# Kernel tuning notes

Hardware: AMD Instinct MI355X
Metric: run time of the kernel (lower is better)

The kernel has to match this reference:

```python
import jax, jax.numpy as jnp
import numpy as np

EMBED_DIMS = 256

def setup_inputs() -> dict:
    key = jax.random.key(0)
    ks = jax.random.split(key, 6)
    C = EMBED_DIMS
    x = jax.random.normal(ks[0], (4, 2048, C), dtype=jnp.float32)
    prev_x = jax.random.normal(ks[1], (4, 2048, C), dtype=jnp.float32)
    s = 1.0 / np.sqrt(C)
    W_qkv = jax.random.uniform(ks[2], (C, 3 * C), dtype=jnp.float32, minval=-s, maxval=s)
    b_qkv = jax.random.uniform(ks[3], (3 * C,), dtype=jnp.float32, minval=-s, maxval=s)
    W_out = jax.random.uniform(ks[4], (C, C), dtype=jnp.float32, minval=-s, maxval=s)
    b_out = jax.random.uniform(ks[5], (C,), dtype=jnp.float32, minval=-s, maxval=s)
    return {"x": x, "prev_x": prev_x, "W_qkv": W_qkv, "b_qkv": b_qkv,
            "W_out": W_out, "b_out": b_out}

def reference(x, prev_x, W_qkv, b_qkv, W_out, b_out):
    B, N, C = x.shape
    xx = jnp.concatenate([prev_x, x], axis=1)          # [B, S, C], S = 2N
    qkv = xx @ W_qkv + b_qkv                            # [B, S, 3C]
    q, k, v = jnp.split(qkv, 3, axis=-1)                # each [B, S, C]
    scale = 1.0 / jnp.sqrt(jnp.asarray(C, dtype=x.dtype))
    attn = jax.nn.softmax(jnp.einsum('bqc,bkc->bqk', q, k) * scale, axis=-1)
    out = jnp.einsum('bqk,bkc->bqc', attn, v)           # [B, S, C]
    out = out @ W_out + b_out
    return out[:, -N:, :]                               # [B, N, C]
```

## Files before the change

kernel.cpp:

```cpp
#include <hip/hip_runtime.h>

typedef __bf16 bf16;
typedef __attribute__((ext_vector_type(8))) __bf16 bf16x8;
typedef __attribute__((ext_vector_type(4))) __bf16 bf16x4;
typedef __attribute__((ext_vector_type(4))) float f32x4;
typedef __attribute__((ext_vector_type(16))) float f32x16;
typedef __attribute__((ext_vector_type(4))) unsigned u32x4;

#define MFMA16(a, b, c) __builtin_amdgcn_mfma_f32_16x16x32_bf16(a, b, c, 0, 0, 0)
#define MFMA32(a, b, c) __builtin_amdgcn_mfma_f32_32x32x16_bf16(a, b, c, 0, 0, 0)

__device__ inline void gload_lds16(const void* g, void* l) {
  __builtin_amdgcn_global_load_lds(
      (const __attribute__((address_space(1))) void*)g,
      (__attribute__((address_space(3))) void*)l, 16, 0, 0);
}

__device__ inline unsigned packbf(float a, float b) {
  unsigned short x = __builtin_bit_cast(unsigned short, (bf16)a);
  unsigned short y = __builtin_bit_cast(unsigned short, (bf16)b);
  return (unsigned)x | ((unsigned)y << 16);
}

__global__ __launch_bounds__(256) void prep_w_kernel(
    const float* __restrict__ Wqkv, const float* __restrict__ Wout,
    bf16* __restrict__ Wqkvt, bf16* __restrict__ Woutt)
{
  int tid = blockIdx.x * 256 + threadIdx.x;
  int nth = gridDim.x * 256;
  for (int i = tid; i < 768 * 256; i += nth) {
    int n = i >> 8, k = i & 255;
    Wqkvt[i] = (bf16)Wqkv[k * 768 + n];
  }
  for (int i = tid; i < 256 * 256; i += nth) {
    int n = i >> 8, k = i & 255;
    Woutt[i] = (bf16)Wout[k * 256 + n];
  }
}

__global__ __launch_bounds__(256) void gemm_qkv_kernel(
    const float* __restrict__ x, const float* __restrict__ px,
    const bf16* __restrict__ Wt, const float* __restrict__ bias,
    bf16* __restrict__ Qo, bf16* __restrict__ KVo)
{
  const int idb = blockIdx.x;
  const int b = idb / 160;
  const int r = idb % 160;
  int mblk, y;
  if (r < 64) { mblk = r >> 2; y = 2 + (r & 3); }
  else { int r2 = r - 64; mblk = 16 + r2 / 6; y = r2 % 6; }
  const int bm = b * 4096 + mblk * 128;
  const int n0 = y * 128;

  const int tid = threadIdx.x;
  const int lane = tid & 63, w = tid >> 6;
  const int l15 = lane & 15, lg = lane >> 4;

  alignas(16) __shared__ bf16 Alds[128 * 32];
  alignas(16) __shared__ bf16 Wlds[128 * 32];

  f32x4 acc[2][8] = {};

  const float* xsrc = ((bm & 4095) < 2048) ? px : x;
  const size_t xbase = ((size_t)b << 19) + (size_t)(bm & 2047) * 256;

  for (int k0 = 0; k0 < 256; k0 += 32) {
    __syncthreads();
    #pragma unroll
    for (int it = 0; it < 2; it++) {
      int c = it * 256 + tid;
      int row = c >> 2, kc = (c & 3) << 3;
      const float* src = xsrc + xbase + (size_t)row * 256 + k0 + kc;
      float4 f0 = *(const float4*)src;
      float4 f1 = *(const float4*)(src + 4);
      bf16x8 v = { (bf16)f0.x, (bf16)f0.y, (bf16)f0.z, (bf16)f0.w,
                   (bf16)f1.x, (bf16)f1.y, (bf16)f1.z, (bf16)f1.w };
      *(bf16x8*)((char*)Alds + ((c << 4) ^ (((row >> 1) & 3) << 4))) = v;
    }
    #pragma unroll
    for (int jj = 0; jj < 2; jj++) {
      int j = w * 2 + jj;
      int row = j * 16 + (lane >> 2);
      int chunk = (lane & 3) ^ ((row >> 1) & 3);
      const bf16* g = Wt + (size_t)(n0 + row) * 256 + k0 + chunk * 8;
      gload_lds16(g, (char*)Wlds + j * 1024);
    }
    __syncthreads();

    const int arow0 = w * 32 + l15;
    bf16x8 af0 = *(const bf16x8*)((char*)Alds +
        (((arow0 << 6) + (lg << 4)) ^ (((arow0 >> 1) & 3) << 4)));
    const int arow1 = arow0 + 16;
    bf16x8 af1 = *(const bf16x8*)((char*)Alds +
        (((arow1 << 6) + (lg << 4)) ^ (((arow1 >> 1) & 3) << 4)));
    #pragma unroll
    for (int nt = 0; nt < 8; nt++) {
      const int wrow = nt * 16 + l15;
      bf16x8 bfr = *(const bf16x8*)((char*)Wlds +
          (((wrow << 6) + (lg << 4)) ^ (((wrow >> 1) & 3) << 4)));
      acc[0][nt] = MFMA16(af0, bfr, acc[0][nt]);
      acc[1][nt] = MFMA16(af1, bfr, acc[1][nt]);
    }
  }

  #pragma unroll
  for (int mt = 0; mt < 2; mt++) {
    #pragma unroll
    for (int nt = 0; nt < 8; nt++) {
      const int n = n0 + nt * 16 + l15;
      const float bv = bias[n];
      const int m0 = bm + w * 32 + mt * 16 + lg * 4;
      const int bq = m0 >> 12;
      const int s = m0 & 4095;
      if (n < 256) {
        if (s >= 2048) {
          const int ks = n >> 4, h2 = (n >> 3) & 1, e = n & 7;
          #pragma unroll
          for (int rr = 0; rr < 4; rr++) {
            const int qrow = bq * 2048 + (s - 2048) + rr;
            Qo[(size_t)(qrow >> 5) * 8192 + ks * 512 +
               ((qrow & 31) + 32 * h2) * 8 + e] =
                (bf16)((acc[mt][nt][rr] + bv) * 0.0625f);
          }
        }
      } else if (n < 512) {
        const int d = n - 256;
        const int ks = d >> 4, h2 = (d >> 3) & 1, e = d & 7;
        const size_t tb = (size_t)(bq * 128 + (s >> 5)) * 16384;
        #pragma unroll
        for (int rr = 0; rr < 4; rr++)
          KVo[tb + ks * 512 + (((s & 31) + rr) + 32 * h2) * 8 + e] =
              (bf16)(acc[mt][nt][rr] + bv);
      } else {
        const int d = n - 512;
        const int kv32 = s & 31;
        const int sidx = kv32 >> 4, h2 = (kv32 >> 3) & 1, e0 = kv32 & 7;
        bf16x4 st = { (bf16)(acc[mt][nt][0] + bv), (bf16)(acc[mt][nt][1] + bv),
                      (bf16)(acc[mt][nt][2] + bv), (bf16)(acc[mt][nt][3] + bv) };
        *(bf16x4*)(KVo + (size_t)(bq * 128 + (s >> 5)) * 16384 + 8192 +
                   (sidx * 8 + (d >> 5)) * 512 + ((d & 31) + 32 * h2) * 8 + e0) = st;
      }
    }
  }
}

__global__ __launch_bounds__(256, 2) void attn_kernel(
    const bf16* __restrict__ Qp, const bf16* __restrict__ KVp,
    bf16* __restrict__ Opart, float* __restrict__ ml)
{
  const int id = blockIdx.x;
  const int c = id & 7;
  const int b = (id >> 3) & 3;
  const int qb = id >> 5;
  const int tid = threadIdx.x;
  const int lane = tid & 63, w = tid >> 6;
  const int l31 = lane & 31, hi = lane >> 5;

  __shared__ bf16 lds[2][16384];

  const int qg = b * 64 + qb * 4 + w;
  const bf16* qbase = Qp + (size_t)qg * 8192 + lane * 8;
  bf16x8 qf[16];
  #pragma unroll
  for (int ks = 0; ks < 16; ks++)
    qf[ks] = *(const bf16x8*)(qbase + ks * 512);

  const bf16* kvtile0 = KVp + (size_t)(b * 128 + c * 16) * 16384;

  auto stage = [&](int t) {
    const char* g = (const char*)(kvtile0 + (size_t)t * 16384) + w * 8192 + lane * 16;
    char* l = (char*)&lds[t & 1][0] + w * 8192;
    #pragma unroll
    for (int j = 0; j < 8; j++)
      gload_lds16(g + j * 1024, l + j * 1024);
  };
  stage(0);

  f32x16 o[8] = {};
  float m_run = -1e30f, l_run = 0.f;

  for (int t = 0; t < 16; t++) {
    __syncthreads();
    if (t + 1 < 16) stage(t + 1);
    const bf16* kbuf = &lds[t & 1][0];
    const bf16* vbuf = kbuf + 8192;

    f32x16 p = {};
    __builtin_amdgcn_s_setprio(1);
    #pragma unroll
    for (int ks = 0; ks < 16; ks++) {
      bf16x8 kf = *(const bf16x8*)(kbuf + ks * 512 + lane * 8);
      p = MFMA32(kf, qf[ks], p);
    }
    __builtin_amdgcn_s_setprio(0);

    float mt = fmaxf(p[0], p[1]);
    #pragma unroll
    for (int i = 2; i < 16; i++) mt = fmaxf(mt, p[i]);
    mt = fmaxf(mt, __shfl_xor(mt, 32));
    if (!__all(mt <= m_run + 8.f)) {
      const float m_new = fmaxf(m_run, mt);
      const float alpha = __expf(m_run - m_new);
      l_run *= alpha;
      #pragma unroll
      for (int i = 0; i < 8; i++)
        #pragma unroll
        for (int j = 0; j < 16; j++) o[i][j] *= alpha;
      m_run = m_new;
    }
    float ps = 0.f;
    #pragma unroll
    for (int i = 0; i < 16; i++) { p[i] = __expf(p[i] - m_run); ps += p[i]; }
    ps += __shfl_xor(ps, 32);
    l_run += ps;

    unsigned u[8], xp[8];
    #pragma unroll
    for (int i = 0; i < 8; i++) u[i] = packbf(p[2 * i], p[2 * i + 1]);
    #pragma unroll
    for (int i = 0; i < 8; i++)
      xp[i] = (unsigned)__shfl_xor((int)u[i], 32);
    const u32x4 w0 = hi ? (u32x4){xp[2], xp[3], u[2], u[3]}
                        : (u32x4){u[0], u[1], xp[0], xp[1]};
    const u32x4 w1 = hi ? (u32x4){xp[6], xp[7], u[6], u[7]}
                        : (u32x4){u[4], u[5], xp[4], xp[5]};
    const bf16x8 pf0 = __builtin_bit_cast(bf16x8, w0);
    const bf16x8 pf1 = __builtin_bit_cast(bf16x8, w1);

    __builtin_amdgcn_s_setprio(1);
    #pragma unroll
    for (int dg = 0; dg < 8; dg++) {
      bf16x8 v0 = *(const bf16x8*)(vbuf + dg * 512 + lane * 8);
      o[dg] = MFMA32(v0, pf0, o[dg]);
      bf16x8 v1 = *(const bf16x8*)(vbuf + (8 + dg) * 512 + lane * 8);
      o[dg] = MFMA32(v1, pf1, o[dg]);
    }
    __builtin_amdgcn_s_setprio(0);
  }

  const int q = b * 2048 + qb * 128 + w * 32 + l31;
  bf16* ob = Opart + ((size_t)c * 8192 + q) * 256;
  #pragma unroll
  for (int dg = 0; dg < 8; dg++) {
    #pragma unroll
    for (int r4 = 0; r4 < 4; r4++) {
      const int d = dg * 32 + r4 * 8 + hi * 4;
      bf16x4 st = { (bf16)o[dg][r4 * 4 + 0], (bf16)o[dg][r4 * 4 + 1],
                    (bf16)o[dg][r4 * 4 + 2], (bf16)o[dg][r4 * 4 + 3] };
      *(bf16x4*)(ob + d) = st;
    }
  }
  if (hi == 0) {
    float2 v = { m_run, l_run };
    *(float2*)(ml + ((size_t)c * 8192 + q) * 2) = v;
  }
}

__global__ __launch_bounds__(256) void out_kernel(
    const bf16* __restrict__ Opart, const float* __restrict__ ml,
    const bf16* __restrict__ Woutt, const float* __restrict__ bout,
    float* __restrict__ out)
{
  const int bm = blockIdx.x * 32;
  const int tid = threadIdx.x;
  const int lane = tid & 63, w = tid >> 6;
  const int l15 = lane & 15, lg = lane >> 4;

  alignas(16) __shared__ bf16 Alds[32 * 256];
  alignas(16) __shared__ bf16 Wlds[2][256 * 32];

  auto stageW = [&](int k0) {
    #pragma unroll
    for (int jj = 0; jj < 4; jj++) {
      int j = w * 4 + jj;
      int row = j * 16 + (lane >> 2);
      int chunk = (lane & 3) ^ ((row >> 1) & 3);
      const bf16* g = Woutt + (size_t)row * 256 + k0 * 32 + chunk * 8;
      gload_lds16(g, (char*)&Wlds[k0 & 1][0] + j * 1024);
    }
  };
  stageW(0);

  #pragma unroll
  for (int ch = 0; ch < 4; ch++) {
    const int idx = ch * 256 + tid;
    const int row = idx >> 5;
    const int dc = (idx & 31) << 3;
    const int q = bm + row;
    float ms[8], ls[8], M = -1e30f;
    #pragma unroll
    for (int s = 0; s < 8; s++) {
      float2 v = *(const float2*)(ml + ((size_t)s * 8192 + q) * 2);
      ms[s] = v.x; ls[s] = v.y;
      M = fmaxf(M, v.x);
    }
    float L = 0.f, acc[8] = {};
    #pragma unroll
    for (int s = 0; s < 8; s++) {
      const float wgt = __expf(ms[s] - M);
      L += ls[s] * wgt;
      bf16x8 v = *(const bf16x8*)(Opart + ((size_t)s * 8192 + q) * 256 + dc);
      #pragma unroll
      for (int j = 0; j < 8; j++) acc[j] += wgt * (float)v[j];
    }
    const float inv = 1.f / L;
    bf16x8 st;
    #pragma unroll
    for (int j = 0; j < 8; j++) st[j] = (bf16)(acc[j] * inv);
    *(bf16x8*)((char*)Alds + ((row * 512 + dc * 2) ^ ((row & 7) << 4))) = st;
  }
  __syncthreads();

  f32x4 acc[8] = {};
  for (int k0 = 0; k0 < 8; k0++) {
    if (k0 + 1 < 8) stageW(k0 + 1);
    const bf16* wbuf = &Wlds[k0 & 1][0];
    const int arow = (w & 1) * 16 + l15;
    bf16x8 afr = *(const bf16x8*)((char*)Alds +
        ((arow * 512 + k0 * 64 + lg * 16) ^ ((arow & 7) << 4)));
    #pragma unroll
    for (int nt = 0; nt < 8; nt++) {
      const int wrow = (w >> 1) * 128 + nt * 16 + l15;
      bf16x8 bfr = *(const bf16x8*)((char*)wbuf +
          (((wrow << 6) + (lg << 4)) ^ (((wrow >> 1) & 3) << 4)));
      acc[nt] = MFMA16(afr, bfr, acc[nt]);
    }
    __syncthreads();
  }

  #pragma unroll
  for (int nt = 0; nt < 8; nt++) {
    const int n = (w >> 1) * 128 + nt * 16 + l15;
    const float bvv = bout[n];
    const int m0 = bm + (w & 1) * 16 + lg * 4;
    #pragma unroll
    for (int r = 0; r < 4; r++)
      out[(size_t)(m0 + r) * 256 + n] = acc[nt][r] + bvv;
  }
}

extern "C" void kernel_launch(void* const* d_in, const int* in_sizes, int n_in,
                              void* d_out, int out_size, void* d_ws, size_t ws_size,
                              hipStream_t stream) {
  const float* x    = (const float*)d_in[0];
  const float* px   = (const float*)d_in[1];
  const float* Wqkv = (const float*)d_in[2];
  const float* bqkv = (const float*)d_in[3];
  const float* Wout = (const float*)d_in[4];
  const float* bout = (const float*)d_in[5];
  float* out = (float*)d_out;

  char* ws = (char*)d_ws;
  bf16* Qp    = (bf16*)(ws);
  bf16* KVp   = (bf16*)(ws + 4194304);
  bf16* Woutt = (bf16*)(ws + 20971520);
  bf16* Wqkvt = (bf16*)(ws + 21102592);
  float* ml   = (float*)(ws + 21495808);
  bf16* Opart = (bf16*)(ws + 22020096);

  prep_w_kernel<<<dim3(128), dim3(256), 0, stream>>>(Wqkv, Wout, Wqkvt, Woutt);
  gemm_qkv_kernel<<<dim3(640), dim3(256), 0, stream>>>(
      x, px, Wqkvt, bqkv, Qp, KVp);
  attn_kernel<<<dim3(512), dim3(256), 0, stream>>>(Qp, KVp, Opart, ml);
  out_kernel<<<dim3(256), dim3(256), 0, stream>>>(Opart, ml, Woutt, bout, out);
}
```

Before: 91.05 us.

## Restructure QKV GEMM to keep full-K A tile resident and stream W double-buffered

The QKV projection kernel now gives each block a 64-row slab of the input, converts it to bf16 once into LDS for the full K=256, and then loops over the 256-wide output column groups (Q/K/V, or only K/V for the prev half). Weight tiles are double-buffered through LDS with async global-to-LDS loads, so the next tile's load overlaps the current MFMAs. This cuts the repeated fp32 input reads and conversions across column blocks and shrinks the grid from 640 to 256 blocks. In exchange it uses much more LDS per block (lower occupancy), has fewer blocks to fill the GPU, and runs a longer serial per-block loop.

Result: slower. 104.7 us (+15.0%).

```diff
diff --git a/kernel.cpp b/kernel.cpp
--- a/kernel.cpp
+++ b/kernel.cpp
@@ -43,102 +43,104 @@
     const bf16* __restrict__ Wt, const float* __restrict__ bias,
     bf16* __restrict__ Qo, bf16* __restrict__ KVo)
 {
-  const int idb = blockIdx.x;
-  const int b = idb / 160;
-  const int r = idb % 160;
-  int mblk, y;
-  if (r < 64) { mblk = r >> 2; y = 2 + (r & 3); }
-  else { int r2 = r - 64; mblk = 16 + r2 / 6; y = r2 % 6; }
-  const int bm = b * 4096 + mblk * 128;
-  const int n0 = y * 128;
+  const int bi = blockIdx.x;
+  const int b = bi >> 6;
+  const int mblk = bi & 63;
+  const bool mhalf = mblk >= 32;
+  const int bm = b * 4096 + mblk * 64;
+  const int s_local = (mblk & 31) * 64;
+  const float* xsrc = mhalf ? x : px;
+  const size_t xbase = ((size_t)b << 19) + (size_t)s_local * 256;
 
   const int tid = threadIdx.x;
   const int lane = tid & 63, w = tid >> 6;
   const int l15 = lane & 15, lg = lane >> 4;
 
-  alignas(16) __shared__ bf16 Alds[128 * 32];
-  alignas(16) __shared__ bf16 Wlds[128 * 32];
-
-  f32x4 acc[2][8] = {};
-
-  const float* xsrc = ((bm & 4095) < 2048) ? px : x;
-  const size_t xbase = ((size_t)b << 19) + (size_t)(bm & 2047) * 256;
-
-  for (int k0 = 0; k0 < 256; k0 += 32) {
-    __syncthreads();
-    #pragma unroll
-    for (int it = 0; it < 2; it++) {
-      int c = it * 256 + tid;
-      int row = c >> 2, kc = (c & 3) << 3;
-      const float* src = xsrc + xbase + (size_t)row * 256 + k0 + kc;
-      float4 f0 = *(const float4*)src;
-      float4 f1 = *(const float4*)(src + 4);
-      bf16x8 v = { (bf16)f0.x, (bf16)f0.y, (bf16)f0.z, (bf16)f0.w,
-                   (bf16)f1.x, (bf16)f1.y, (bf16)f1.z, (bf16)f1.w };
-      *(bf16x8*)((char*)Alds + ((c << 4) ^ (((row >> 1) & 3) << 4))) = v;
-    }
-    #pragma unroll
-    for (int jj = 0; jj < 2; jj++) {
-      int j = w * 2 + jj;
+  alignas(16) __shared__ bf16 Alds[64 * 256];
+  alignas(16) __shared__ bf16 Wlds[2][256 * 32];
+
+  const int ystart = mhalf ? 0 : 1;
+  const int nseq = mhalf ? 24 : 16;
+
+  auto stageW = [&](int i) {
+    const int y = ystart + (i >> 3);
+    const int k0 = (i & 7) * 32;
+    #pragma unroll
+    for (int jj = 0; jj < 4; jj++) {
+      int j = w * 4 + jj;
       int row = j * 16 + (lane >> 2);
       int chunk = (lane & 3) ^ ((row >> 1) & 3);
-      const bf16* g = Wt + (size_t)(n0 + row) * 256 + k0 + chunk * 8;
-      gload_lds16(g, (char*)Wlds + j * 1024);
+      const bf16* g = Wt + (size_t)(y * 256 + row) * 256 + k0 + chunk * 8;
+      gload_lds16(g, (char*)&Wlds[i & 1][0] + j * 1024);
+    }
+  };
+  stageW(0);
+
+  #pragma unroll
+  for (int it = 0; it < 8; it++) {
+    int c = it * 256 + tid;
+    int row = c >> 5, ch = c & 31;
+    const float* src = xsrc + xbase + (size_t)row * 256 + ch * 8;
+    float4 f0 = *(const float4*)src;
+    float4 f1 = *(const float4*)(src + 4);
+    bf16x8 v = { (bf16)f0.x, (bf16)f0.y, (bf16)f0.z, (bf16)f0.w,
+                 (bf16)f1.x, (bf16)f1.y, (bf16)f1.z, (bf16)f1.w };
+    *(bf16x8*)((char*)Alds + ((c << 4) ^ ((row & 7) << 4))) = v;
+  }
+  __syncthreads();
+
+  f32x4 acc[16] = {};
+  for (int i = 0; i < nseq; i++) {
+    if (i + 1 < nseq) stageW(i + 1);
+    const int k0 = (i & 7) * 32;
+    const bf16* wbuf = &Wlds[i & 1][0];
+    const int arow = w * 16 + l15;
+    bf16x8 afr = *(const bf16x8*)((char*)Alds +
+        ((arow * 512 + k0 * 2 + lg * 16) ^ ((arow & 7) << 4)));
+    #pragma unroll
+    for (int nt = 0; nt < 16; nt++) {
+      const int wrow = nt * 16 + l15;
+      bf16x8 bfr = *(const bf16x8*)((char*)wbuf +
+          (((wrow << 6) + (lg << 4)) ^ (((wrow >> 1) & 3) << 4)));
+      acc[nt] = MFMA16(afr, bfr, acc[nt]);
     }
     __syncthreads();
 
-    const int arow0 = w * 32 + l15;
-    bf16x8 af0 = *(const bf16x8*)((char*)Alds +
-        (((arow0 << 6) + (lg << 4)) ^ (((arow0 >> 1) & 3) << 4)));
-    const int arow1 = arow0 + 16;
-    bf16x8 af1 = *(const bf16x8*)((char*)Alds +
-        (((arow1 << 6) + (lg << 4)) ^ (((arow1 >> 1) & 3) << 4)));
-    #pragma unroll
-    for (int nt = 0; nt < 8; nt++) {
-      const int wrow = nt * 16 + l15;
-      bf16x8 bfr = *(const bf16x8*)((char*)Wlds +
-          (((wrow << 6) + (lg << 4)) ^ (((wrow >> 1) & 3) << 4)));
-      acc[0][nt] = MFMA16(af0, bfr, acc[0][nt]);
-      acc[1][nt] = MFMA16(af1, bfr, acc[1][nt]);
-    }
-  }
-
-  #pragma unroll
-  for (int mt = 0; mt < 2; mt++) {
-    #pragma unroll
-    for (int nt = 0; nt < 8; nt++) {
-      const int n = n0 + nt * 16 + l15;
-      const float bv = bias[n];
-      const int m0 = bm + w * 32 + mt * 16 + lg * 4;
-      const int bq = m0 >> 12;
-      const int s = m0 & 4095;
-      if (n < 256) {
-        if (s >= 2048) {
+    if ((i & 7) == 7) {
+      const int y = ystart + (i >> 3);
+      const int m0 = bm + w * 16 + lg * 4;
+      const int bq = m0 >> 12, s = m0 & 4095;
+      #pragma unroll
+      for (int nt = 0; nt < 16; nt++) {
+        const int n = nt * 16 + l15;
+        const float bv = bias[y * 256 + n];
+        if (y == 0) {
           const int ks = n >> 4, h2 = (n >> 3) & 1, e = n & 7;
           #pragma unroll
           for (int rr = 0; rr < 4; rr++) {
             const int qrow = bq * 2048 + (s - 2048) + rr;
             Qo[(size_t)(qrow >> 5) * 8192 + ks * 512 +
                ((qrow & 31) + 32 * h2) * 8 + e] =
-                (bf16)((acc[mt][nt][rr] + bv) * 0.0625f);
+                (bf16)((acc[nt][rr] + bv) * 0.0625f);
           }
+        } else if (y == 1) {
+          const int d = n;
+          const int ks = d >> 4, h2 = (d >> 3) & 1, e = d & 7;
+          const size_t tb = (size_t)(bq * 128 + (s >> 5)) * 16384;
+          #pragma unroll
+          for (int rr = 0; rr < 4; rr++)
+            KVo[tb + ks * 512 + (((s & 31) + rr) + 32 * h2) * 8 + e] =
+                (bf16)(acc[nt][rr] + bv);
+        } else {
+          const int d = n;
+          const int kv32 = s & 31;
+          const int sidx = kv32 >> 4, h2 = (kv32 >> 3) & 1, e0 = kv32 & 7;
+          bf16x4 st = { (bf16)(acc[nt][0] + bv), (bf16)(acc[nt][1] + bv),
+                        (bf16)(acc[nt][2] + bv), (bf16)(acc[nt][3] + bv) };
+          *(bf16x4*)(KVo + (size_t)(bq * 128 + (s >> 5)) * 16384 + 8192 +
+                     (sidx * 8 + (d >> 5)) * 512 + ((d & 31) + 32 * h2) * 8 + e0) = st;
         }
-      } else if (n < 512) {
-        const int d = n - 256;
-        const int ks = d >> 4, h2 = (d >> 3) & 1, e = d & 7;
-        const size_t tb = (size_t)(bq * 128 + (s >> 5)) * 16384;
-        #pragma unroll
-        for (int rr = 0; rr < 4; rr++)
-          KVo[tb + ks * 512 + (((s & 31) + rr) + 32 * h2) * 8 + e] =
-              (bf16)(acc[mt][nt][rr] + bv);
-      } else {
-        const int d = n - 512;
-        const int kv32 = s & 31;
-        const int sidx = kv32 >> 4, h2 = (kv32 >> 3) & 1, e0 = kv32 & 7;
-        bf16x4 st = { (bf16)(acc[mt][nt][0] + bv), (bf16)(acc[mt][nt][1] + bv),
-                      (bf16)(acc[mt][nt][2] + bv), (bf16)(acc[mt][nt][3] + bv) };
-        *(bf16x4*)(KVo + (size_t)(bq * 128 + (s >> 5)) * 16384 + 8192 +
-                   (sidx * 8 + (d >> 5)) * 512 + ((d & 31) + 32 * h2) * 8 + e0) = st;
+        acc[nt] = (f32x4){};
       }
     }
   }
@@ -359,7 +361,7 @@
   bf16* Opart = (bf16*)(ws + 22020096);
 
   prep_w_kernel<<<dim3(128), dim3(256), 0, stream>>>(Wqkv, Wout, Wqkvt, Woutt);
-  gemm_qkv_kernel<<<dim3(640), dim3(256), 0, stream>>>(
+  gemm_qkv_kernel<<<dim3(256), dim3(256), 0, stream>>>(
       x, px, Wqkvt, bqkv, Qp, KVp);
   attn_kernel<<<dim3(512), dim3(256), 0, stream>>>(Qp, KVp, Opart, ml);
   out_kernel<<<dim3(256), dim3(256), 0, stream>>>(Opart, ml, Woutt, bout, out);
```
